# Kernel tuning notes

Hardware: AMD Instinct MI355X
Metric: run time of the kernel (lower is better)

Reference implementation:

```python
import jax, jax.numpy as jnp
import numpy as np

N = 50000      # nodes
E = 640000     # edges
D = 128        # input/hidden dim
L = 3          # GIN layers
G = 256        # graphs in batch
LAT = 64       # latent dim
BN_EPS = 1e-5
SLOPE = 0.2    # LeakyReLU negative slope


def _leaky(h):
    return jnp.where(h >= 0, h, SLOPE * h)


def setup_inputs() -> dict:
    key = jax.random.key(0)
    ks = jax.random.split(key, 8)
    x = jax.random.normal(ks[0], (N, D), dtype=jnp.float32)
    edge_index = jax.random.randint(ks[1], (2, E), 0, N, dtype=jnp.int64)
    batch = jnp.sort(jax.random.randint(ks[2], (N,), 0, G, dtype=jnp.int64))
    W1 = jax.random.normal(ks[3], (L, D, D), dtype=jnp.float32) * 0.05
    W2 = jax.random.normal(ks[4], (L, D, D), dtype=jnp.float32) * 0.05
    fc_W = jax.random.normal(ks[5], (LAT, D), dtype=jnp.float32) * 0.05
    return {
        "x": x,
        "W1": W1,
        "b1": jnp.zeros((L, D), jnp.float32),
        "bn_g": jnp.ones((L, D), jnp.float32),
        "bn_b": jnp.zeros((L, D), jnp.float32),
        "bn_m": jnp.zeros((L, D), jnp.float32),
        "bn_v": jax.random.uniform(ks[6], (L, D), jnp.float32, 0.5, 1.5),
        "W2": W2,
        "b2": jnp.zeros((L, D), jnp.float32),
        "out_g": jnp.ones((D,), jnp.float32),
        "out_b": jnp.zeros((D,), jnp.float32),
        "out_m": jnp.zeros((D,), jnp.float32),
        "out_v": jax.random.uniform(ks[7], (D,), jnp.float32, 0.5, 1.5),
        "fc_W": fc_W,
        "fc_b": jnp.zeros((LAT,), jnp.float32),
        "edge_index": edge_index,
        "batch": batch,
    }


def reference(x, W1, b1, bn_g, bn_b, bn_m, bn_v, W2, b2,
              out_g, out_b, out_m, out_v, fc_W, fc_b,
              edge_index, batch):
    src, dst = edge_index[0], edge_index[1]
    for i in range(L):
        # GINConv: (1+eps)*x + sum_{j in N(i)} x_j  (eps=0 default)
        agg = x + jax.ops.segment_sum(x[src], dst, num_segments=N)
        # MLP: Linear -> LeakyReLU -> BatchNorm(eval) -> Linear -> LeakyReLU
        h = _leaky(agg @ W1[i].T + b1[i])
        h = (h - bn_m[i]) * jax.lax.rsqrt(bn_v[i] + BN_EPS) * bn_g[i] + bn_b[i]
        x = _leaky(h @ W2[i].T + b2[i])
        # dropout is identity in eval mode
    pooled = jax.ops.segment_sum(x, batch, num_segments=G)  # [G, D]
    out = (pooled - out_m) * jax.lax.rsqrt(out_v + BN_EPS) * out_g + out_b
    return out @ fc_W.T + fc_b  # [G, LAT]
```

## Files before the change

kernel.cpp:

```cpp
#include <hip/hip_runtime.h>
#include <cstdint>
#include <cstddef>

#define NN 50000
#define EE 640000
#define DD 128
#define LL 3
#define GG 256
#define LATD 64

typedef __attribute__((ext_vector_type(8))) __bf16 bf16x8;
typedef __attribute__((ext_vector_type(4))) float f32x4;

__device__ __forceinline__ unsigned short f2bf(float f) {
  __bf16 h = (__bf16)f;
  return __builtin_bit_cast(unsigned short, h);
}
__device__ __forceinline__ float bf2f(unsigned int u16) {
  unsigned int x = u16 << 16;
  return __builtin_bit_cast(float, x);
}
__device__ __forceinline__ void unpack8(uint4 v, float* f) {
  f[0] = bf2f(v.x & 0xffffu); f[1] = bf2f(v.x >> 16);
  f[2] = bf2f(v.y & 0xffffu); f[3] = bf2f(v.y >> 16);
  f[4] = bf2f(v.z & 0xffffu); f[5] = bf2f(v.z >> 16);
  f[6] = bf2f(v.w & 0xffffu); f[7] = bf2f(v.w >> 16);
}

__global__ __launch_bounds__(256) void cvt_kernel(const float4* __restrict__ x,
                                                  uint4* __restrict__ xb, int n8) {
  int t = blockIdx.x * 256 + threadIdx.x;
  if (t >= n8) return;
  float4 a = x[t * 2], b = x[t * 2 + 1];
  uint4 v;
  v.x = f2bf(a.x) | ((unsigned)f2bf(a.y) << 16);
  v.y = f2bf(a.z) | ((unsigned)f2bf(a.w) << 16);
  v.z = f2bf(b.x) | ((unsigned)f2bf(b.y) << 16);
  v.w = f2bf(b.z) | ((unsigned)f2bf(b.w) << 16);
  xb[t] = v;
}

__global__ __launch_bounds__(256) void hist_kernel(const int* __restrict__ dst,
                                                   int* __restrict__ counts, int E) {
  int e = blockIdx.x * blockDim.x + threadIdx.x;
  if (e < E) atomicAdd(&counts[dst[e]], 1);
}

__global__ __launch_bounds__(256) void scan1_kernel(const int* __restrict__ counts,
                                                    int* __restrict__ rp,
                                                    int* __restrict__ bsum, int n) {
  int i = blockIdx.x * 256 + threadIdx.x;
  int v = (i < n) ? counts[i] : 0;
  int lane = threadIdx.x & 63, w = threadIdx.x >> 6;
  int s = v;
#pragma unroll
  for (int off = 1; off < 64; off <<= 1) {
    int u = __shfl_up(s, off);
    if (lane >= off) s += u;
  }
  __shared__ int ws[4];
  if (lane == 63) ws[w] = s;
  __syncthreads();
  int add = 0;
#pragma unroll
  for (int k = 0; k < 4; ++k) if (k < w) add += ws[k];
  int incl = s + add;
  if (i < n) rp[i] = incl - v;
  if (threadIdx.x == 255) bsum[blockIdx.x] = incl;
}

__global__ __launch_bounds__(256) void scan2_kernel(int* __restrict__ bsum, int nb) {
  int t = threadIdx.x;
  int v = (t < nb) ? bsum[t] : 0;
  int lane = t & 63, w = t >> 6;
  int s = v;
#pragma unroll
  for (int off = 1; off < 64; off <<= 1) {
    int u = __shfl_up(s, off);
    if (lane >= off) s += u;
  }
  __shared__ int ws[4];
  if (lane == 63) ws[w] = s;
  __syncthreads();
  int add = 0;
#pragma unroll
  for (int k = 0; k < 4; ++k) if (k < w) add += ws[k];
  int incl = s + add;
  if (t < nb) bsum[t] = incl - v;
}

__global__ __launch_bounds__(256) void scan3_kernel(int* __restrict__ rp,
                                                    int* __restrict__ cursor,
                                                    const int* __restrict__ bsum, int n) {
  int i = blockIdx.x * 256 + threadIdx.x;
  if (i < n) {
    int v = rp[i] + bsum[blockIdx.x];
    rp[i] = v;
    cursor[i] = v;
  }
  if (i == 0) rp[n] = EE;
}

__global__ __launch_bounds__(256) void fill_kernel(const int* __restrict__ src,
                                                   const int* __restrict__ dst,
                                                   int* __restrict__ cursor,
                                                   int* __restrict__ col, int E) {
  int e = blockIdx.x * blockDim.x + threadIdx.x;
  if (e < E) {
    int p = atomicAdd(&cursor[dst[e]], 1);
    col[p] = src[e];
  }
}

__global__ __launch_bounds__(256) void agg_kernel(const uint4* __restrict__ xin,
                                                  const int* __restrict__ row_ptr,
                                                  const int* __restrict__ col,
                                                  uint4* __restrict__ agg, int n) {
  int tid = blockIdx.x * 256 + threadIdx.x;
  int node = tid >> 4;
  int c = tid & 15;
  if (node >= n) return;
  float acc[8], tmp[8];
  unpack8(xin[(size_t)node * 16 + c], acc);
  int s = row_ptr[node], e = row_ptr[node + 1];
  for (int j = s; j < e; ++j) {
    int sc = col[j];
    unpack8(xin[(size_t)sc * 16 + c], tmp);
#pragma unroll
    for (int i = 0; i < 8; ++i) acc[i] += tmp[i];
  }
  uint4 v;
  v.x = f2bf(acc[0]) | ((unsigned)f2bf(acc[1]) << 16);
  v.y = f2bf(acc[2]) | ((unsigned)f2bf(acc[3]) << 16);
  v.z = f2bf(acc[4]) | ((unsigned)f2bf(acc[5]) << 16);
  v.w = f2bf(acc[6]) | ((unsigned)f2bf(acc[7]) << 16);
  agg[(size_t)node * 16 + c] = v;
}

#define SWZ(byte_, row_) ((byte_) ^ (((row_) & 7) << 4))

__global__ __launch_bounds__(512, 2) void mlp_mfma(
    const unsigned short* __restrict__ agg, unsigned short* __restrict__ xout,
    const float* __restrict__ W1, const float* __restrict__ b1,
    const float* __restrict__ bng, const float* __restrict__ bnb,
    const float* __restrict__ bnm, const float* __restrict__ bnv,
    const float* __restrict__ W2, const float* __restrict__ b2, int n) {
  __shared__ __align__(16) char smem[131072];
  char* w1p = smem;
  char* w2p = smem + 32768;
  char* xp  = smem + 65536;

#pragma unroll
  for (int it = 0; it < 8; ++it) {
    int chunk = it * 512 + threadIdx.x;
    int row = chunk >> 5, k4 = chunk & 31;
    int byte = SWZ(row * 256 + k4 * 8, row);
    float4 f = ((const float4*)W1)[chunk];
    *(uint2*)(w1p + byte) = make_uint2(
        f2bf(f.x) | ((unsigned)f2bf(f.y) << 16),
        f2bf(f.z) | ((unsigned)f2bf(f.w) << 16));
    float4 g = ((const float4*)W2)[chunk];
    *(uint2*)(w2p + byte) = make_uint2(
        f2bf(g.x) | ((unsigned)f2bf(g.y) << 16),
        f2bf(g.z) | ((unsigned)f2bf(g.w) << 16));
  }
  int base = blockIdx.x * 256;
#pragma unroll
  for (int it = 0; it < 8; ++it) {
    int chunk = it * 512 + threadIdx.x;
    int row = chunk >> 4, kc = chunk & 15;
    int grow = base + row;
    uint4 v = make_uint4(0, 0, 0, 0);
    if (grow < n) v = ((const uint4*)agg)[(size_t)grow * 16 + kc];
    *(uint4*)(xp + SWZ(row * 256 + kc * 16, row)) = v;
  }
  __syncthreads();

  int lane = threadIdx.x & 63;
  int c = lane & 15;
  int half = lane >> 4;
  int wave = threadIdx.x >> 6;
  int Rw = wave * 32;

  float b1v[8], sv[8], tv[8], b2v[8];
#pragma unroll
  for (int ni = 0; ni < 8; ++ni) {
    int cc = ni * 16 + c;
    b1v[ni] = b1[cc];
    float s = bng[cc] * rsqrtf(bnv[cc] + 1e-5f);
    sv[ni] = s;
    tv[ni] = bnb[cc] - bnm[cc] * s;
    b2v[ni] = b2[cc];
  }

  f32x4 acc[2][8];
#pragma unroll
  for (int mi = 0; mi < 2; ++mi)
#pragma unroll
    for (int ni = 0; ni < 8; ++ni) acc[mi][ni] = (f32x4){0.f, 0.f, 0.f, 0.f};

#pragma unroll
  for (int ks = 0; ks < 4; ++ks) {
    bf16x8 a[2];
#pragma unroll
    for (int mi = 0; mi < 2; ++mi) {
      int row = Rw + mi * 16 + c;
      a[mi] = *(const bf16x8*)(xp + SWZ(row * 256 + ks * 64 + half * 16, row));
    }
#pragma unroll
    for (int ni = 0; ni < 8; ++ni) {
      int wr = ni * 16 + c;
      bf16x8 bf = *(const bf16x8*)(w1p + SWZ(wr * 256 + ks * 64 + half * 16, wr));
      acc[0][ni] = __builtin_amdgcn_mfma_f32_16x16x32_bf16(a[0], bf, acc[0][ni], 0, 0, 0);
      acc[1][ni] = __builtin_amdgcn_mfma_f32_16x16x32_bf16(a[1], bf, acc[1][ni], 0, 0, 0);
    }
  }

#pragma unroll
  for (int mi = 0; mi < 2; ++mi)
#pragma unroll
    for (int ni = 0; ni < 8; ++ni)
#pragma unroll
      for (int r = 0; r < 4; ++r) {
        float h = acc[mi][ni][r] + b1v[ni];
        h = h >= 0.f ? h : 0.2f * h;
        h = h * sv[ni] + tv[ni];
        int row = Rw + mi * 16 + half * 4 + r;
        int colb = (ni * 16 + c) * 2;
        *(__bf16*)(xp + SWZ(row * 256 + colb, row)) = (__bf16)h;
      }
  __syncthreads();

#pragma unroll
  for (int mi = 0; mi < 2; ++mi)
#pragma unroll
    for (int ni = 0; ni < 8; ++ni) acc[mi][ni] = (f32x4){0.f, 0.f, 0.f, 0.f};

#pragma unroll
  for (int ks = 0; ks < 4; ++ks) {
    bf16x8 a[2];
#pragma unroll
    for (int mi = 0; mi < 2; ++mi) {
      int row = Rw + mi * 16 + c;
      a[mi] = *(const bf16x8*)(xp + SWZ(row * 256 + ks * 64 + half * 16, row));
    }
#pragma unroll
    for (int ni = 0; ni < 8; ++ni) {
      int wr = ni * 16 + c;
      bf16x8 bf = *(const bf16x8*)(w2p + SWZ(wr * 256 + ks * 64 + half * 16, wr));
      acc[0][ni] = __builtin_amdgcn_mfma_f32_16x16x32_bf16(a[0], bf, acc[0][ni], 0, 0, 0);
      acc[1][ni] = __builtin_amdgcn_mfma_f32_16x16x32_bf16(a[1], bf, acc[1][ni], 0, 0, 0);
    }
  }

#pragma unroll
  for (int mi = 0; mi < 2; ++mi)
#pragma unroll
    for (int ni = 0; ni < 8; ++ni)
#pragma unroll
      for (int r = 0; r < 4; ++r) {
        float xo = acc[mi][ni][r] + b2v[ni];
        xo = xo >= 0.f ? xo : 0.2f * xo;
        int grow = base + Rw + mi * 16 + half * 4 + r;
        if (grow < n) xout[(size_t)grow * DD + ni * 16 + c] = f2bf(xo);
      }
}

__global__ __launch_bounds__(256) void pool_kernel(const uint4* __restrict__ x,
                                                   const int* __restrict__ batch,
                                                   float* __restrict__ pooled, int n) {
  int gid = blockIdx.x * 256 + threadIdx.x;
  int grp = gid >> 4, c = gid & 15;
  int n0 = grp * 16;
  if (n0 >= n) return;
  float acc[8] = {0.f, 0.f, 0.f, 0.f, 0.f, 0.f, 0.f, 0.f};
  int curg = batch[n0];
  int end = n0 + 16 < n ? n0 + 16 : n;
  for (int node = n0; node < end; ++node) {
    int g = batch[node];
    if (g != curg) {
      float* p = pooled + (size_t)curg * DD + c * 8;
#pragma unroll
      for (int i = 0; i < 8; ++i) { atomicAdd(p + i, acc[i]); acc[i] = 0.f; }
      curg = g;
    }
    float tmp[8];
    unpack8(x[(size_t)node * 16 + c], tmp);
#pragma unroll
    for (int i = 0; i < 8; ++i) acc[i] += tmp[i];
  }
  float* p = pooled + (size_t)curg * DD + c * 8;
#pragma unroll
  for (int i = 0; i < 8; ++i) atomicAdd(p + i, acc[i]);
}

__global__ __launch_bounds__(128) void head_kernel(const float* __restrict__ pooled,
    const float* __restrict__ og, const float* __restrict__ ob,
    const float* __restrict__ om, const float* __restrict__ ov,
    const float* __restrict__ fcW, const float* __restrict__ fcb,
    float* __restrict__ out) {
  __shared__ float pb[DD];
  int g = blockIdx.x;
  int t = threadIdx.x;
  float s = og[t] * rsqrtf(ov[t] + 1e-5f);
  pb[t] = (pooled[(size_t)g * DD + t] - om[t]) * s + ob[t];
  __syncthreads();
  if (t < LATD) {
    float acc = fcb[t];
#pragma unroll 8
    for (int d = 0; d < DD; ++d) acc = fmaf(fcW[t * DD + d], pb[d], acc);
    out[(size_t)g * LATD + t] = acc;
  }
}

extern "C" void kernel_launch(void* const* d_in, const int* in_sizes, int n_in,
                              void* d_out, int out_size, void* d_ws, size_t ws_size,
                              hipStream_t stream) {
  const float* x   = (const float*)d_in[0];
  const float* W1  = (const float*)d_in[1];
  const float* b1  = (const float*)d_in[2];
  const float* bng = (const float*)d_in[3];
  const float* bnb = (const float*)d_in[4];
  const float* bnm = (const float*)d_in[5];
  const float* bnv = (const float*)d_in[6];
  const float* W2  = (const float*)d_in[7];
  const float* b2  = (const float*)d_in[8];
  const float* og  = (const float*)d_in[9];
  const float* ob  = (const float*)d_in[10];
  const float* om  = (const float*)d_in[11];
  const float* ov  = (const float*)d_in[12];
  const float* fcW = (const float*)d_in[13];
  const float* fcb = (const float*)d_in[14];
  const int* ei    = (const int*)d_in[15];
  const int* batch = (const int*)d_in[16];
  const int* src  = ei;
  const int* dstp = ei + EE;

  char* ws = (char*)d_ws;
  size_t off = 0;
  auto alloc = [&](size_t bytes) {
    void* p = ws + off;
    off += (bytes + 255) & ~(size_t)255;
    return p;
  };
  unsigned short* xb0  = (unsigned short*)alloc((size_t)NN * DD * 2);
  unsigned short* xb1  = (unsigned short*)alloc((size_t)NN * DD * 2);
  unsigned short* aggb = (unsigned short*)alloc((size_t)NN * DD * 2);
  int* row_ptr  = (int*)alloc((NN + 1) * 4);
  int* cursor   = (int*)alloc(NN * 4);
  int* counts   = (int*)alloc(NN * 4);
  int* col      = (int*)alloc(EE * 4);
  int* bsum     = (int*)alloc(256 * 4);
  float* pooled = (float*)alloc(GG * DD * 4);

  hipMemsetAsync(counts, 0, NN * 4, stream);
  hipMemsetAsync(pooled, 0, GG * DD * 4, stream);

  cvt_kernel<<<(NN * DD / 8 + 255) / 256, 256, 0, stream>>>(
      (const float4*)x, (uint4*)xb0, NN * DD / 8);

  const int NB = (NN + 255) / 256;
  hist_kernel<<<(EE + 255) / 256, 256, 0, stream>>>(dstp, counts, EE);
  scan1_kernel<<<NB, 256, 0, stream>>>(counts, row_ptr, bsum, NN);
  scan2_kernel<<<1, 256, 0, stream>>>(bsum, NB);
  scan3_kernel<<<NB, 256, 0, stream>>>(row_ptr, cursor, bsum, NN);
  fill_kernel<<<(EE + 255) / 256, 256, 0, stream>>>(src, dstp, cursor, col, EE);

  unsigned short* xcur = xb0;
  unsigned short* xnext = xb1;
  for (int i = 0; i < LL; ++i) {
    agg_kernel<<<(NN * 16 + 255) / 256, 256, 0, stream>>>(
        (const uint4*)xcur, row_ptr, col, (uint4*)aggb, NN);
    mlp_mfma<<<NB, 512, 0, stream>>>(
        aggb, xnext,
        W1 + (size_t)i * DD * DD, b1 + i * DD,
        bng + i * DD, bnb + i * DD, bnm + i * DD, bnv + i * DD,
        W2 + (size_t)i * DD * DD, b2 + i * DD, NN);
    unsigned short* t = xcur; xcur = xnext; xnext = t;
  }
  pool_kernel<<<(NN * 16 + 255) / 256, 256, 0, stream>>>(
      (const uint4*)xcur, batch, pooled, NN);
  head_kernel<<<GG, 128, 0, stream>>>(pooled, og, ob, om, ov, fcW, fcb, (float*)d_out);
}
```

Before: 264.5 us.

## Fuse neighbor aggregation into MLP kernel and pre-convert weights once

Merges the per-layer gather-sum aggregation into the MFMA MLP kernel, so the aggregated features go straight into shared memory and the bf16 agg buffer round trip through global memory disappears. Weights for all layers are converted to swizzled bf16 once in a combined prep kernel, which also absorbs the x conversion and the degree histogram, cutting launches. Blocks shrink to 64 rows and 256 threads, which means more blocks and more weight reloads into LDS (64KB per block). The neighbor loop is unrolled by two to raise memory-level parallelism.

```diff
diff --git a/kernel.cpp b/kernel.cpp
--- a/kernel.cpp
+++ b/kernel.cpp
@@ -26,24 +26,49 @@
   f[4] = bf2f(v.z & 0xffffu); f[5] = bf2f(v.z >> 16);
   f[6] = bf2f(v.w & 0xffffu); f[7] = bf2f(v.w >> 16);
 }
-
-__global__ __launch_bounds__(256) void cvt_kernel(const float4* __restrict__ x,
-                                                  uint4* __restrict__ xb, int n8) {
-  int t = blockIdx.x * 256 + threadIdx.x;
-  if (t >= n8) return;
-  float4 a = x[t * 2], b = x[t * 2 + 1];
+__device__ __forceinline__ uint4 pack8(const float* f) {
   uint4 v;
-  v.x = f2bf(a.x) | ((unsigned)f2bf(a.y) << 16);
-  v.y = f2bf(a.z) | ((unsigned)f2bf(a.w) << 16);
-  v.z = f2bf(b.x) | ((unsigned)f2bf(b.y) << 16);
-  v.w = f2bf(b.z) | ((unsigned)f2bf(b.w) << 16);
-  xb[t] = v;
-}
-
-__global__ __launch_bounds__(256) void hist_kernel(const int* __restrict__ dst,
-                                                   int* __restrict__ counts, int E) {
-  int e = blockIdx.x * blockDim.x + threadIdx.x;
-  if (e < E) atomicAdd(&counts[dst[e]], 1);
+  v.x = f2bf(f[0]) | ((unsigned)f2bf(f[1]) << 16);
+  v.y = f2bf(f[2]) | ((unsigned)f2bf(f[3]) << 16);
+  v.z = f2bf(f[4]) | ((unsigned)f2bf(f[5]) << 16);
+  v.w = f2bf(f[6]) | ((unsigned)f2bf(f[7]) << 16);
+  return v;
+}
+
+#define SWZ(byte_, row_) ((byte_) ^ (((row_) & 7) << 4))
+
+#define CVT_BLK 3125
+#define WCV_BLK 48
+#define HIST_BLK 2500
+__global__ __launch_bounds__(256) void prep_kernel(
+    const float4* __restrict__ x, uint4* __restrict__ xb,
+    const float* __restrict__ W1, const float* __restrict__ W2,
+    uint4* __restrict__ wb, const int* __restrict__ dst,
+    int* __restrict__ counts) {
+  int b = blockIdx.x;
+  if (b < CVT_BLK) {
+    int t = b * 256 + threadIdx.x;
+    float4 a = x[t * 2], bb = x[t * 2 + 1];
+    float f[8] = {a.x, a.y, a.z, a.w, bb.x, bb.y, bb.z, bb.w};
+    xb[t] = pack8(f);
+  } else if (b < CVT_BLK + WCV_BLK) {
+    int t = (b - CVT_BLK) * 256 + threadIdx.x;
+    int m = t >> 11;
+    int q = t & 2047;
+    int byte = q * 16;
+    int row = byte >> 8;
+    int inner = byte & 255;
+    int isrc = inner ^ ((row & 7) << 4);
+    int k0 = isrc >> 1;
+    const float* Wsrc = (m & 1) ? W2 : W1;
+    const float* p = Wsrc + ((size_t)(m >> 1) * DD * DD + row * DD + k0);
+    float4 f0 = ((const float4*)p)[0], f1 = ((const float4*)p)[1];
+    float f[8] = {f0.x, f0.y, f0.z, f0.w, f1.x, f1.y, f1.z, f1.w};
+    wb[(size_t)m * 2048 + q] = pack8(f);
+  } else {
+    int e = (b - CVT_BLK - WCV_BLK) * 256 + threadIdx.x;
+    atomicAdd(&counts[dst[e]], 1);
+  }
 }
 
 __global__ __launch_bounds__(256) void scan1_kernel(const int* __restrict__ counts,
@@ -112,75 +137,63 @@
   }
 }
 
-__global__ __launch_bounds__(256) void agg_kernel(const uint4* __restrict__ xin,
-                                                  const int* __restrict__ row_ptr,
-                                                  const int* __restrict__ col,
-                                                  uint4* __restrict__ agg, int n) {
-  int tid = blockIdx.x * 256 + threadIdx.x;
-  int node = tid >> 4;
-  int c = tid & 15;
-  if (node >= n) return;
-  float acc[8], tmp[8];
-  unpack8(xin[(size_t)node * 16 + c], acc);
-  int s = row_ptr[node], e = row_ptr[node + 1];
-  for (int j = s; j < e; ++j) {
-    int sc = col[j];
-    unpack8(xin[(size_t)sc * 16 + c], tmp);
-#pragma unroll
-    for (int i = 0; i < 8; ++i) acc[i] += tmp[i];
-  }
-  uint4 v;
-  v.x = f2bf(acc[0]) | ((unsigned)f2bf(acc[1]) << 16);
-  v.y = f2bf(acc[2]) | ((unsigned)f2bf(acc[3]) << 16);
-  v.z = f2bf(acc[4]) | ((unsigned)f2bf(acc[5]) << 16);
-  v.w = f2bf(acc[6]) | ((unsigned)f2bf(acc[7]) << 16);
-  agg[(size_t)node * 16 + c] = v;
-}
-
-#define SWZ(byte_, row_) ((byte_) ^ (((row_) & 7) << 4))
-
-__global__ __launch_bounds__(512, 2) void mlp_mfma(
-    const unsigned short* __restrict__ agg, unsigned short* __restrict__ xout,
-    const float* __restrict__ W1, const float* __restrict__ b1,
-    const float* __restrict__ bng, const float* __restrict__ bnb,
-    const float* __restrict__ bnm, const float* __restrict__ bnv,
-    const float* __restrict__ W2, const float* __restrict__ b2, int n) {
-  __shared__ __align__(16) char smem[131072];
+__global__ __launch_bounds__(256) void gin_layer(
+    const uint4* __restrict__ xin, unsigned short* __restrict__ xout,
+    const uint4* __restrict__ w1b, const uint4* __restrict__ w2b,
+    const float* __restrict__ b1, const float* __restrict__ bng,
+    const float* __restrict__ bnb, const float* __restrict__ bnm,
+    const float* __restrict__ bnv, const float* __restrict__ b2,
+    const int* __restrict__ row_ptr, const int* __restrict__ colv, int n) {
+  __shared__ __align__(16) char smem[81920];
   char* w1p = smem;
   char* w2p = smem + 32768;
   char* xp  = smem + 65536;
 
 #pragma unroll
   for (int it = 0; it < 8; ++it) {
-    int chunk = it * 512 + threadIdx.x;
-    int row = chunk >> 5, k4 = chunk & 31;
-    int byte = SWZ(row * 256 + k4 * 8, row);
-    float4 f = ((const float4*)W1)[chunk];
-    *(uint2*)(w1p + byte) = make_uint2(
-        f2bf(f.x) | ((unsigned)f2bf(f.y) << 16),
-        f2bf(f.z) | ((unsigned)f2bf(f.w) << 16));
-    float4 g = ((const float4*)W2)[chunk];
-    *(uint2*)(w2p + byte) = make_uint2(
-        f2bf(g.x) | ((unsigned)f2bf(g.y) << 16),
-        f2bf(g.z) | ((unsigned)f2bf(g.w) << 16));
-  }
-  int base = blockIdx.x * 256;
-#pragma unroll
-  for (int it = 0; it < 8; ++it) {
-    int chunk = it * 512 + threadIdx.x;
-    int row = chunk >> 4, kc = chunk & 15;
-    int grow = base + row;
-    uint4 v = make_uint4(0, 0, 0, 0);
-    if (grow < n) v = ((const uint4*)agg)[(size_t)grow * 16 + kc];
-    *(uint4*)(xp + SWZ(row * 256 + kc * 16, row)) = v;
+    int q = it * 256 + threadIdx.x;
+    ((uint4*)w1p)[q] = w1b[q];
+    ((uint4*)w2p)[q] = w2b[q];
+  }
+
+  int base = blockIdx.x * 64;
+#pragma unroll
+  for (int it = 0; it < 4; ++it) {
+    int t = it * 256 + threadIdx.x;
+    int row = t >> 4, c = t & 15;
+    int node = base + row;
+    float acc[8];
+    if (node < n) {
+      unpack8(xin[(size_t)node * 16 + c], acc);
+      int s = row_ptr[node], e = row_ptr[node + 1];
+      int j = s;
+      for (; j + 1 < e; j += 2) {
+        int n0 = colv[j], n1 = colv[j + 1];
+        float t0[8], t1[8];
+        unpack8(xin[(size_t)n0 * 16 + c], t0);
+        unpack8(xin[(size_t)n1 * 16 + c], t1);
+#pragma unroll
+        for (int i = 0; i < 8; ++i) acc[i] += t0[i] + t1[i];
+      }
+      if (j < e) {
+        float t0[8];
+        unpack8(xin[(size_t)colv[j] * 16 + c], t0);
+#pragma unroll
+        for (int i = 0; i < 8; ++i) acc[i] += t0[i];
+      }
+    } else {
+#pragma unroll
+      for (int i = 0; i < 8; ++i) acc[i] = 0.f;
+    }
+    *(uint4*)(xp + SWZ(row * 256 + c * 16, row)) = pack8(acc);
   }
   __syncthreads();
 
   int lane = threadIdx.x & 63;
   int c = lane & 15;
-  int half = lane >> 4;
+  int kq = lane >> 4;
   int wave = threadIdx.x >> 6;
-  int Rw = wave * 32;
+  int r0 = wave * 16;
 
   float b1v[8], sv[8], tv[8], b2v[8];
 #pragma unroll
@@ -193,77 +206,58 @@
     b2v[ni] = b2[cc];
   }
 
-  f32x4 acc[2][8];
-#pragma unroll
-  for (int mi = 0; mi < 2; ++mi)
-#pragma unroll
-    for (int ni = 0; ni < 8; ++ni) acc[mi][ni] = (f32x4){0.f, 0.f, 0.f, 0.f};
+  f32x4 acc[8];
+#pragma unroll
+  for (int ni = 0; ni < 8; ++ni) acc[ni] = (f32x4){0.f, 0.f, 0.f, 0.f};
 
 #pragma unroll
   for (int ks = 0; ks < 4; ++ks) {
-    bf16x8 a[2];
-#pragma unroll
-    for (int mi = 0; mi < 2; ++mi) {
-      int row = Rw + mi * 16 + c;
-      a[mi] = *(const bf16x8*)(xp + SWZ(row * 256 + ks * 64 + half * 16, row));
-    }
+    int row = r0 + c;
+    bf16x8 a = *(const bf16x8*)(xp + SWZ(row * 256 + ks * 64 + kq * 16, row));
 #pragma unroll
     for (int ni = 0; ni < 8; ++ni) {
       int wr = ni * 16 + c;
-      bf16x8 bf = *(const bf16x8*)(w1p + SWZ(wr * 256 + ks * 64 + half * 16, wr));
-      acc[0][ni] = __builtin_amdgcn_mfma_f32_16x16x32_bf16(a[0], bf, acc[0][ni], 0, 0, 0);
-      acc[1][ni] = __builtin_amdgcn_mfma_f32_16x16x32_bf16(a[1], bf, acc[1][ni], 0, 0, 0);
-    }
-  }
-
-#pragma unroll
-  for (int mi = 0; mi < 2; ++mi)
-#pragma unroll
-    for (int ni = 0; ni < 8; ++ni)
-#pragma unroll
-      for (int r = 0; r < 4; ++r) {
-        float h = acc[mi][ni][r] + b1v[ni];
-        h = h >= 0.f ? h : 0.2f * h;
-        h = h * sv[ni] + tv[ni];
-        int row = Rw + mi * 16 + half * 4 + r;
-        int colb = (ni * 16 + c) * 2;
-        *(__bf16*)(xp + SWZ(row * 256 + colb, row)) = (__bf16)h;
-      }
-  __syncthreads();
-
-#pragma unroll
-  for (int mi = 0; mi < 2; ++mi)
-#pragma unroll
-    for (int ni = 0; ni < 8; ++ni) acc[mi][ni] = (f32x4){0.f, 0.f, 0.f, 0.f};
+      bf16x8 bfr = *(const bf16x8*)(w1p + SWZ(wr * 256 + ks * 64 + kq * 16, wr));
+      acc[ni] = __builtin_amdgcn_mfma_f32_16x16x32_bf16(a, bfr, acc[ni], 0, 0, 0);
+    }
+  }
+
+#pragma unroll
+  for (int ni = 0; ni < 8; ++ni)
+#pragma unroll
+    for (int r = 0; r < 4; ++r) {
+      float h = acc[ni][r] + b1v[ni];
+      h = h >= 0.f ? h : 0.2f * h;
+      h = h * sv[ni] + tv[ni];
+      int row = r0 + kq * 4 + r;
+      *(__bf16*)(xp + SWZ(row * 256 + (ni * 16 + c) * 2, row)) = (__bf16)h;
+    }
+  __syncthreads();
+
+#pragma unroll
+  for (int ni = 0; ni < 8; ++ni) acc[ni] = (f32x4){0.f, 0.f, 0.f, 0.f};
 
 #pragma unroll
   for (int ks = 0; ks < 4; ++ks) {
-    bf16x8 a[2];
-#pragma unroll
-    for (int mi = 0; mi < 2; ++mi) {
-      int row = Rw + mi * 16 + c;
-      a[mi] = *(const bf16x8*)(xp + SWZ(row * 256 + ks * 64 + half * 16, row));
-    }
+    int row = r0 + c;
+    bf16x8 a = *(const bf16x8*)(xp + SWZ(row * 256 + ks * 64 + kq * 16, row));
 #pragma unroll
     for (int ni = 0; ni < 8; ++ni) {
       int wr = ni * 16 + c;
-      bf16x8 bf = *(const bf16x8*)(w2p + SWZ(wr * 256 + ks * 64 + half * 16, wr));
-      acc[0][ni] = __builtin_amdgcn_mfma_f32_16x16x32_bf16(a[0], bf, acc[0][ni], 0, 0, 0);
-      acc[1][ni] = __builtin_amdgcn_mfma_f32_16x16x32_bf16(a[1], bf, acc[1][ni], 0, 0, 0);
-    }
-  }
-
-#pragma unroll
-  for (int mi = 0; mi < 2; ++mi)
-#pragma unroll
-    for (int ni = 0; ni < 8; ++ni)
-#pragma unroll
-      for (int r = 0; r < 4; ++r) {
-        float xo = acc[mi][ni][r] + b2v[ni];
-        xo = xo >= 0.f ? xo : 0.2f * xo;
-        int grow = base + Rw + mi * 16 + half * 4 + r;
-        if (grow < n) xout[(size_t)grow * DD + ni * 16 + c] = f2bf(xo);
-      }
+      bf16x8 bfr = *(const bf16x8*)(w2p + SWZ(wr * 256 + ks * 64 + kq * 16, wr));
+      acc[ni] = __builtin_amdgcn_mfma_f32_16x16x32_bf16(a, bfr, acc[ni], 0, 0, 0);
+    }
+  }
+
+#pragma unroll
+  for (int ni = 0; ni < 8; ++ni)
+#pragma unroll
+    for (int r = 0; r < 4; ++r) {
+      float xo = acc[ni][r] + b2v[ni];
+      xo = xo >= 0.f ? xo : 0.2f * xo;
+      int grow = base + r0 + kq * 4 + r;
+      if (grow < n) xout[(size_t)grow * DD + ni * 16 + c] = f2bf(xo);
+    }
 }
 
 __global__ __launch_bounds__(256) void pool_kernel(const uint4* __restrict__ x,
@@ -345,7 +339,7 @@
   };
   unsigned short* xb0  = (unsigned short*)alloc((size_t)NN * DD * 2);
   unsigned short* xb1  = (unsigned short*)alloc((size_t)NN * DD * 2);
-  unsigned short* aggb = (unsigned short*)alloc((size_t)NN * DD * 2);
+  uint4* wb     = (uint4*)alloc((size_t)6 * 2048 * 16);
   int* row_ptr  = (int*)alloc((NN + 1) * 4);
   int* cursor   = (int*)alloc(NN * 4);
   int* counts   = (int*)alloc(NN * 4);
@@ -356,11 +350,10 @@
   hipMemsetAsync(counts, 0, NN * 4, stream);
   hipMemsetAsync(pooled, 0, GG * DD * 4, stream);
 
-  cvt_kernel<<<(NN * DD / 8 + 255) / 256, 256, 0, stream>>>(
-      (const float4*)x, (uint4*)xb0, NN * DD / 8);
+  prep_kernel<<<CVT_BLK + WCV_BLK + HIST_BLK, 256, 0, stream>>>(
+      (const float4*)x, (uint4*)xb0, W1, W2, wb, dstp, counts);
 
   const int NB = (NN + 255) / 256;
-  hist_kernel<<<(EE + 255) / 256, 256, 0, stream>>>(dstp, counts, EE);
   scan1_kernel<<<NB, 256, 0, stream>>>(counts, row_ptr, bsum, NN);
   scan2_kernel<<<1, 256, 0, stream>>>(bsum, NB);
   scan3_kernel<<<NB, 256, 0, stream>>>(row_ptr, cursor, bsum, NN);
@@ -368,14 +361,13 @@
 
   unsigned short* xcur = xb0;
   unsigned short* xnext = xb1;
+  const int GB = (NN + 63) / 64;
   for (int i = 0; i < LL; ++i) {
-    agg_kernel<<<(NN * 16 + 255) / 256, 256, 0, stream>>>(
-        (const uint4*)xcur, row_ptr, col, (uint4*)aggb, NN);
-    mlp_mfma<<<NB, 512, 0, stream>>>(
-        aggb, xnext,
-        W1 + (size_t)i * DD * DD, b1 + i * DD,
-        bng + i * DD, bnb + i * DD, bnm + i * DD, bnv + i * DD,
-        W2 + (size_t)i * DD * DD, b2 + i * DD, NN);
+    gin_layer<<<GB, 256, 0, stream>>>(
+        (const uint4*)xcur, xnext,
+        wb + (size_t)i * 4096, wb + (size_t)i * 4096 + 2048,
+        b1 + i * DD, bng + i * DD, bnb + i * DD, bnm + i * DD, bnv + i * DD,
+        b2 + i * DD, row_ptr, col, NN);
     unsigned short* t = xcur; xcur = xnext; xnext = t;
   }
   pool_kernel<<<(NN * 16 + 255) / 256, 256, 0, stream>>>(
```

Measured after the change: 322.9 us. 1.22x slower.
